# Performance work log

Measured on AMD Instinct MI355X. Metric: run time of the kernel, lower is better.

Reference implementation:

```python
import jax, jax.numpy as jnp
import numpy as np

EMBED_DIM = 1024
NUM_HEADS = 16
HEAD_DIM = EMBED_DIM // NUM_HEADS


def setup_inputs() -> dict:
    key = jax.random.key(0)
    k_x, k_wqkv, k_bqkv, k_wo, k_bo = jax.random.split(key, 5)
    B, T, C = 8, 1024, EMBED_DIM
    s = 1.0 / np.sqrt(C)
    return {
        "x": jax.random.normal(k_x, (B, T, C), dtype=jnp.float32),
        "W_qkv": jax.random.uniform(k_wqkv, (C, 3 * C), minval=-s, maxval=s, dtype=jnp.float32),
        "b_qkv": jax.random.uniform(k_bqkv, (3 * C,), minval=-s, maxval=s, dtype=jnp.float32),
        "W_out": jax.random.uniform(k_wo, (C, C), minval=-s, maxval=s, dtype=jnp.float32),
        "b_out": jax.random.uniform(k_bo, (C,), minval=-s, maxval=s, dtype=jnp.float32),
    }


def reference(x, W_qkv, b_qkv, W_out, b_out):
    B, T, C = x.shape
    H, D = NUM_HEADS, HEAD_DIM
    qkv = x @ W_qkv + b_qkv                      # [B,T,3C]
    q, k, v = jnp.split(qkv, 3, axis=-1)
    q = q.reshape(B, T, H, D).transpose(0, 2, 1, 3)  # [B,H,T,D]
    k = k.reshape(B, T, H, D).transpose(0, 2, 1, 3)
    v = v.reshape(B, T, H, D).transpose(0, 2, 1, 3)
    scores = jnp.einsum("bhqd,bhkd->bhqk", q, k) / np.sqrt(D).astype(np.float32)
    causal = jnp.tril(jnp.ones((T, T), dtype=bool))
    scores = jnp.where(causal[None, None], scores, -jnp.inf)
    attn = jax.nn.softmax(scores, axis=-1)       # dropout is identity in eval
    out = jnp.einsum("bhqk,bhkd->bhqd", attn, v)
    out = out.transpose(0, 2, 1, 3).reshape(B, T, C)
    return out @ W_out + b_out
```

## Files before the change

### kernel.cpp

```cpp
#include <hip/hip_runtime.h>
#include <hip/hip_bf16.h>
#include <cstdint>

using bf16 = __hip_bfloat16;
typedef short short8 __attribute__((ext_vector_type(8)));
typedef float floatx4 __attribute__((ext_vector_type(4)));

__device__ __forceinline__ void async_load16(const bf16* g, bf16* l) {
    __builtin_amdgcn_global_load_lds(
        (const __attribute__((address_space(1))) uint32_t*)g,
        (__attribute__((address_space(3))) uint32_t*)l, 16, 0, 0);
}

__device__ __forceinline__ uint32_t pack2(float a, float b) {
    union { bf16 h[2]; uint32_t u; } p;
    p.h[0] = __float2bfloat16(a);
    p.h[1] = __float2bfloat16(b);
    return p.u;
}

__global__ __launch_bounds__(256)
void cvt_bf16_kernel(const float* __restrict__ in, bf16* __restrict__ out) {
    const int i = (blockIdx.x * 256 + threadIdx.x) * 4;
    const float4 v = *(const float4*)(in + i);
    bf16 o[4] = {__float2bfloat16(v.x), __float2bfloat16(v.y),
                 __float2bfloat16(v.z), __float2bfloat16(v.w)};
    *(ushort4*)(out + i) = *(ushort4*)o;
}

__global__ __launch_bounds__(256)
void transpose_cvt_kernel(const float* __restrict__ in, bf16* __restrict__ out,
                          int R, int C) {
    __shared__ float tile[32][33];
    const int tx = threadIdx.x & 31, ty = threadIdx.x >> 5;
    const int c0 = blockIdx.x * 32, r0 = blockIdx.y * 32;
    #pragma unroll
    for (int i = 0; i < 32; i += 8)
        tile[ty + i][tx] = in[(size_t)(r0 + ty + i) * C + c0 + tx];
    __syncthreads();
    #pragma unroll
    for (int i = 0; i < 32; i += 8)
        out[(size_t)(c0 + ty + i) * R + r0 + tx] = __float2bfloat16(tile[tx][ty + i]);
}

template <int MODE>
__global__ __launch_bounds__(256, 2)
void gemm_bt_kernel(const bf16* __restrict__ A, const bf16* __restrict__ Bt,
                    const float* __restrict__ bias, int K,
                    bf16* __restrict__ q_ws, bf16* __restrict__ k_ws,
                    bf16* __restrict__ vt_ws, float* __restrict__ out, int N) {
    __shared__ bf16 As[128 * 32];
    __shared__ bf16 Bs[128 * 32];
    const int tid = threadIdx.x;
    const int wave = tid >> 6, lane = tid & 63;
    const int ln = lane & 15, quad = lane >> 4;
    const int wm = wave & 1, wn = wave >> 1;
    const int m0 = blockIdx.y * 128, n0 = blockIdx.x * 128;

    floatx4 acc[4][4] = {};

    for (int k0 = 0; k0 < K; k0 += 32) {
        __syncthreads();
        #pragma unroll
        for (int c = 0; c < 2; ++c) {
            const int e = (c * 256 + tid) * 8;
            async_load16(A + (size_t)(m0 + (e >> 5)) * K + k0 + (e & 31),
                         &As[(c * 256 + wave * 64) * 8]);
        }
        #pragma unroll
        for (int c = 0; c < 2; ++c) {
            const int e = (c * 256 + tid) * 8;
            async_load16(Bt + (size_t)(n0 + (e >> 5)) * K + k0 + (e & 31),
                         &Bs[(c * 256 + wave * 64) * 8]);
        }
        __syncthreads();

        short8 af[4], bfr[4];
        #pragma unroll
        for (int i = 0; i < 4; ++i) {
            af[i]  = *(const short8*)&As[(wm * 64 + i * 16 + ln) * 32 + quad * 8];
            bfr[i] = *(const short8*)&Bs[(wn * 64 + i * 16 + ln) * 32 + quad * 8];
        }
        #pragma unroll
        for (int mi = 0; mi < 4; ++mi)
            #pragma unroll
            for (int ni = 0; ni < 4; ++ni)
                acc[mi][ni] = __builtin_amdgcn_mfma_f32_16x16x32_bf16(
                    af[mi], bfr[ni], acc[mi][ni], 0, 0, 0);
    }

    #pragma unroll
    for (int ni = 0; ni < 4; ++ni) {
        const int col = n0 + wn * 64 + ni * 16 + ln;
        const float bv = bias[col];
        if (MODE == 0) {
            const int which = col >> 10;
            const int cc = col & 1023;
            const int h = cc >> 6, d = cc & 63;
            #pragma unroll
            for (int mi = 0; mi < 4; ++mi) {
                const int rowb = m0 + wm * 64 + mi * 16 + quad * 4;
                if (which == 2) {
                    const int bb = rowb >> 10, t = rowb & 1023;
                    const int tl = t & 63;
                    const int tt = (t & ~63) + ((((tl >> 3) ^ (d & 7)) << 3) | (tl & 7));
                    uint2 w2 = { pack2(acc[mi][ni][0] + bv, acc[mi][ni][1] + bv),
                                 pack2(acc[mi][ni][2] + bv, acc[mi][ni][3] + bv) };
                    *(uint2*)&vt_ws[((size_t)(bb * 16 + h) * 64 + d) * 1024 + tt] = w2;
                } else {
                    bf16* dst = (which == 0) ? q_ws : k_ws;
                    #pragma unroll
                    for (int r = 0; r < 4; ++r) {
                        const int row = rowb + r;
                        const int bb = row >> 10, t = row & 1023;
                        float v = acc[mi][ni][r] + bv;
                        if (which == 0) v *= 0.1803368801111601f;
                        const int dd = (((d >> 3) ^ (t & 7)) << 3) | (d & 7);
                        dst[((size_t)(bb * 16 + h) * 1024 + t) * 64 + dd] =
                            __float2bfloat16(v);
                    }
                }
            }
        } else {
            #pragma unroll
            for (int mi = 0; mi < 4; ++mi) {
                const int rowb = m0 + wm * 64 + mi * 16 + quad * 4;
                #pragma unroll
                for (int r = 0; r < 4; ++r)
                    out[(size_t)(rowb + r) * N + col] = acc[mi][ni][r] + bv;
            }
        }
    }
}

__global__ __launch_bounds__(256, 3)
void attn_kernel(const bf16* __restrict__ Q, const bf16* __restrict__ K,
                 const bf16* __restrict__ Vt, bf16* __restrict__ O) {
    constexpr int T = 1024;
    __shared__ bf16 Qs[128 * 64];
    __shared__ bf16 Ks[64 * 64];
    __shared__ bf16 Vts[64 * 64];
    __shared__ bf16 Ps[128 * 64];

    const int jt = blockIdx.x;
    const int q0 = jt * 128;
    const int bh = blockIdx.y;
    const int tid = threadIdx.x;
    const int wave = tid >> 6, lane = tid & 63;
    const int ln = lane & 15, quad = lane >> 4;

    const bf16* Qg = Q + (size_t)bh * T * 64 + (size_t)q0 * 64;
    const bf16* Kg = K + (size_t)bh * T * 64;
    const bf16* Vg = Vt + (size_t)bh * 64 * T;

    #pragma unroll
    for (int c = 0; c < 4; ++c)
        async_load16(Qg + (size_t)(c * 256 + tid) * 8, &Qs[(c * 256 + wave * 64) * 8]);
    __syncthreads();

    short8 bq[2][2];
    #pragma unroll
    for (int qj = 0; qj < 2; ++qj)
        #pragma unroll
        for (int ks = 0; ks < 2; ++ks) {
            const int row = wave * 32 + qj * 16 + ln;
            const int ch = (ks * 4 + quad) ^ (row & 7);
            bq[qj][ks] = *(const short8*)&Qs[row * 64 + ch * 8];
        }

    floatx4 oacc[4][2] = {};
    float rm[2] = {-1e30f, -1e30f}, rl[2] = {0.f, 0.f};
    const int qbw = q0 + wave * 32;

    const int nkt = 2 * jt + 2;
    for (int kt = 0; kt < nkt; ++kt) {
        __syncthreads();
        #pragma unroll
        for (int c = 0; c < 2; ++c)
            async_load16(Kg + (size_t)kt * 4096 + (size_t)(c * 256 + tid) * 8,
                         &Ks[(c * 256 + wave * 64) * 8]);
        #pragma unroll
        for (int c = 0; c < 2; ++c) {
            const int e = (c * 256 + tid) * 8;
            async_load16(Vg + (size_t)(e >> 6) * T + kt * 64 + (e & 63),
                         &Vts[(c * 256 + wave * 64) * 8]);
        }
        __syncthreads();

        const int k0 = kt * 64;
        if (k0 > qbw + 31) continue;
        const bool tail = (k0 + 63 > qbw);

        floatx4 sacc[4][2] = {};
        #pragma unroll
        for (int nj = 0; nj < 4; ++nj) {
            if (tail && k0 + nj * 16 > qbw + 31) continue;
            short8 ak[2];
            #pragma unroll
            for (int ks = 0; ks < 2; ++ks) {
                const int row = nj * 16 + ln;
                const int ch = (ks * 4 + quad) ^ (row & 7);
                ak[ks] = *(const short8*)&Ks[row * 64 + ch * 8];
            }
            #pragma unroll
            for (int qj = 0; qj < 2; ++qj) {
                if (tail && k0 + nj * 16 > qbw + qj * 16 + 15) continue;
                #pragma unroll
                for (int ks = 0; ks < 2; ++ks)
                    sacc[nj][qj] = __builtin_amdgcn_mfma_f32_16x16x32_bf16(
                        ak[ks], bq[qj][ks], sacc[nj][qj], 0, 0, 0);
            }
        }

        if (tail) {
            #pragma unroll
            for (int nj = 0; nj < 4; ++nj)
                #pragma unroll
                for (int qj = 0; qj < 2; ++qj) {
                    const int qq = qbw + qj * 16 + ln;
                    #pragma unroll
                    for (int r = 0; r < 4; ++r) {
                        const int kk = k0 + nj * 16 + quad * 4 + r;
                        if (kk > qq) sacc[nj][qj][r] = -1e30f;
                    }
                }
        }

        #pragma unroll
        for (int qj = 0; qj < 2; ++qj) {
            float mx = sacc[0][qj][0];
            #pragma unroll
            for (int nj = 0; nj < 4; ++nj)
                #pragma unroll
                for (int r = 0; r < 4; ++r) mx = fmaxf(mx, sacc[nj][qj][r]);
            mx = fmaxf(mx, __shfl_xor(mx, 16, 64));
            mx = fmaxf(mx, __shfl_xor(mx, 32, 64));
            const float mn = fmaxf(rm[qj], mx);
            const float alpha = exp2f(rm[qj] - mn);
            rm[qj] = mn;
            rl[qj] *= alpha;
            #pragma unroll
            for (int dt = 0; dt < 4; ++dt) oacc[dt][qj] *= alpha;
            float rs = 0.f;
            const int qrow = wave * 32 + qj * 16 + ln;
            #pragma unroll
            for (int nj = 0; nj < 4; ++nj) {
                float p[4];
                #pragma unroll
                for (int r = 0; r < 4; ++r) {
                    p[r] = exp2f(sacc[nj][qj][r] - mn);
                    rs += p[r];
                }
                const int kcol = nj * 16 + quad * 4;
                const int ch = (kcol >> 3) ^ (qrow & 7);
                uint2 w2 = { pack2(p[0], p[1]), pack2(p[2], p[3]) };
                *(uint2*)&Ps[qrow * 64 + ch * 8 + (kcol & 7)] = w2;
            }
            rl[qj] += rs;
        }

        #pragma unroll
        for (int ks4 = 0; ks4 < 2; ++ks4) {
            short8 bp[2];
            #pragma unroll
            for (int qj = 0; qj < 2; ++qj) {
                const int qrow = wave * 32 + qj * 16 + ln;
                const int ch = (ks4 * 4 + quad) ^ (qrow & 7);
                bp[qj] = *(const short8*)&Ps[qrow * 64 + ch * 8];
            }
            #pragma unroll
            for (int dt = 0; dt < 4; ++dt) {
                const int row = dt * 16 + ln;
                const int ch = (ks4 * 4 + quad) ^ (row & 7);
                const short8 av = *(const short8*)&Vts[row * 64 + ch * 8];
                #pragma unroll
                for (int qj = 0; qj < 2; ++qj)
                    oacc[dt][qj] = __builtin_amdgcn_mfma_f32_16x16x32_bf16(
                        av, bp[qj], oacc[dt][qj], 0, 0, 0);
            }
        }
    }

    const int b = bh >> 4, h = bh & 15;
    #pragma unroll
    for (int qj = 0; qj < 2; ++qj) {
        float l = rl[qj];
        l += __shfl_xor(l, 16, 64);
        l += __shfl_xor(l, 32, 64);
        const float inv = 1.0f / l;
        const int t = q0 + wave * 32 + qj * 16 + ln;
        const size_t rowb = ((size_t)b * 1024 + t) * 1024 + h * 64;
        #pragma unroll
        for (int dt = 0; dt < 4; ++dt) {
            uint2 w2 = { pack2(oacc[dt][qj][0] * inv, oacc[dt][qj][1] * inv),
                         pack2(oacc[dt][qj][2] * inv, oacc[dt][qj][3] * inv) };
            *(uint2*)&O[rowb + dt * 16 + quad * 4] = w2;
        }
    }
}

extern "C" void kernel_launch(void* const* d_in, const int* in_sizes, int n_in,
                              void* d_out, int out_size, void* d_ws, size_t ws_size,
                              hipStream_t stream) {
    const float* x     = (const float*)d_in[0];
    const float* W_qkv = (const float*)d_in[1];
    const float* b_qkv = (const float*)d_in[2];
    const float* W_out = (const float*)d_in[3];
    const float* b_out = (const float*)d_in[4];
    float* out = (float*)d_out;

    char* ws = (char*)d_ws;
    const size_t MB = 1u << 20;
    bf16* x_bf   = (bf16*)(ws + 0);
    bf16* wqkv_t = (bf16*)(ws + 16 * MB);
    bf16* wout_t = (bf16*)(ws + 22 * MB);
    bf16* q_ws   = (bf16*)(ws + 24 * MB);
    bf16* k_ws   = (bf16*)(ws + 40 * MB);
    bf16* vt_ws  = (bf16*)(ws + 56 * MB);
    bf16* ao_ws  = (bf16*)(ws + 72 * MB);

    cvt_bf16_kernel<<<8192, 256, 0, stream>>>(x, x_bf);
    transpose_cvt_kernel<<<dim3(96, 32), 256, 0, stream>>>(W_qkv, wqkv_t, 1024, 3072);
    transpose_cvt_kernel<<<dim3(32, 32), 256, 0, stream>>>(W_out, wout_t, 1024, 1024);

    gemm_bt_kernel<0><<<dim3(24, 64), 256, 0, stream>>>(
        x_bf, wqkv_t, b_qkv, 1024, q_ws, k_ws, vt_ws, nullptr, 3072);

    attn_kernel<<<dim3(8, 128), 256, 0, stream>>>(q_ws, k_ws, vt_ws, ao_ws);

    gemm_bt_kernel<1><<<dim3(8, 64), 256, 0, stream>>>(
        ao_ws, wout_t, b_out, 1024, nullptr, nullptr, nullptr, out, 1024);
}
```

Baseline: 286.2 us.

## Pair causal query tiles per block and double-buffer K/V tiles in attention

Each attention block now handles two query tiles, jt and 7-jt, so the causal work per block is balanced and the grid is halved. K and V tiles are double-buffered so the next tile's async global-to-LDS load is issued before computing on the current one, leaving one barrier per iteration. The Q staging buffer is reused for the P tile, which offsets the extra LDS used by the second K/V buffers. With fewer blocks, there is less parallelism to hide latency, and each block runs twice as long.

```diff
diff --git a/kernel.cpp b/kernel.cpp
--- a/kernel.cpp
+++ b/kernel.cpp
@@ -137,164 +137,183 @@
 void attn_kernel(const bf16* __restrict__ Q, const bf16* __restrict__ K,
                  const bf16* __restrict__ Vt, bf16* __restrict__ O) {
     constexpr int T = 1024;
-    __shared__ bf16 Qs[128 * 64];
-    __shared__ bf16 Ks[64 * 64];
-    __shared__ bf16 Vts[64 * 64];
-    __shared__ bf16 Ps[128 * 64];
-
-    const int jt = blockIdx.x;
-    const int q0 = jt * 128;
+    __shared__ bf16 QPs[128 * 64];
+    __shared__ bf16 Ks[2][64 * 64];
+    __shared__ bf16 Vts[2][64 * 64];
+
     const int bh = blockIdx.y;
     const int tid = threadIdx.x;
     const int wave = tid >> 6, lane = tid & 63;
     const int ln = lane & 15, quad = lane >> 4;
 
-    const bf16* Qg = Q + (size_t)bh * T * 64 + (size_t)q0 * 64;
     const bf16* Kg = K + (size_t)bh * T * 64;
     const bf16* Vg = Vt + (size_t)bh * 64 * T;
+    const int b = bh >> 4, h = bh & 15;
 
     #pragma unroll
-    for (int c = 0; c < 4; ++c)
-        async_load16(Qg + (size_t)(c * 256 + tid) * 8, &Qs[(c * 256 + wave * 64) * 8]);
-    __syncthreads();
-
-    short8 bq[2][2];
-    #pragma unroll
-    for (int qj = 0; qj < 2; ++qj)
-        #pragma unroll
-        for (int ks = 0; ks < 2; ++ks) {
-            const int row = wave * 32 + qj * 16 + ln;
-            const int ch = (ks * 4 + quad) ^ (row & 7);
-            bq[qj][ks] = *(const short8*)&Qs[row * 64 + ch * 8];
-        }
-
-    floatx4 oacc[4][2] = {};
-    float rm[2] = {-1e30f, -1e30f}, rl[2] = {0.f, 0.f};
-    const int qbw = q0 + wave * 32;
-
-    const int nkt = 2 * jt + 2;
-    for (int kt = 0; kt < nkt; ++kt) {
-        __syncthreads();
+    for (int phase = 0; phase < 2; ++phase) {
+        const int jt = phase ? 7 - blockIdx.x : blockIdx.x;
+        const int q0 = jt * 128;
+        const int nkt = 2 * jt + 2;
+
+        const bf16* Qg = Q + (size_t)bh * T * 64 + (size_t)q0 * 64;
+        #pragma unroll
+        for (int c = 0; c < 4; ++c)
+            async_load16(Qg + (size_t)(c * 256 + tid) * 8,
+                         &QPs[(c * 256 + wave * 64) * 8]);
         #pragma unroll
         for (int c = 0; c < 2; ++c)
-            async_load16(Kg + (size_t)kt * 4096 + (size_t)(c * 256 + tid) * 8,
-                         &Ks[(c * 256 + wave * 64) * 8]);
+            async_load16(Kg + (size_t)(c * 256 + tid) * 8,
+                         &Ks[0][(c * 256 + wave * 64) * 8]);
         #pragma unroll
         for (int c = 0; c < 2; ++c) {
             const int e = (c * 256 + tid) * 8;
-            async_load16(Vg + (size_t)(e >> 6) * T + kt * 64 + (e & 63),
-                         &Vts[(c * 256 + wave * 64) * 8]);
+            async_load16(Vg + (size_t)(e >> 6) * T + (e & 63),
+                         &Vts[0][(c * 256 + wave * 64) * 8]);
         }
         __syncthreads();
 
-        const int k0 = kt * 64;
-        if (k0 > qbw + 31) continue;
-        const bool tail = (k0 + 63 > qbw);
-
-        floatx4 sacc[4][2] = {};
-        #pragma unroll
-        for (int nj = 0; nj < 4; ++nj) {
-            if (tail && k0 + nj * 16 > qbw + 31) continue;
-            short8 ak[2];
+        short8 bq[2][2];
+        #pragma unroll
+        for (int qj = 0; qj < 2; ++qj)
             #pragma unroll
             for (int ks = 0; ks < 2; ++ks) {
-                const int row = nj * 16 + ln;
+                const int row = wave * 32 + qj * 16 + ln;
                 const int ch = (ks * 4 + quad) ^ (row & 7);
-                ak[ks] = *(const short8*)&Ks[row * 64 + ch * 8];
-            }
-            #pragma unroll
-            for (int qj = 0; qj < 2; ++qj) {
-                if (tail && k0 + nj * 16 > qbw + qj * 16 + 15) continue;
-                #pragma unroll
-                for (int ks = 0; ks < 2; ++ks)
-                    sacc[nj][qj] = __builtin_amdgcn_mfma_f32_16x16x32_bf16(
-                        ak[ks], bq[qj][ks], sacc[nj][qj], 0, 0, 0);
-            }
-        }
-
-        if (tail) {
-            #pragma unroll
-            for (int nj = 0; nj < 4; ++nj)
+                bq[qj][ks] = *(const short8*)&QPs[row * 64 + ch * 8];
+            }
+
+        floatx4 oacc[4][2] = {};
+        float rm[2] = {-1e30f, -1e30f}, rl[2] = {0.f, 0.f};
+        const int qbw = q0 + wave * 32;
+
+        for (int kt = 0; kt < nkt; ++kt) {
+            const int cur = kt & 1;
+            if (kt + 1 < nkt) {
+                const int nxt = cur ^ 1;
+                #pragma unroll
+                for (int c = 0; c < 2; ++c)
+                    async_load16(Kg + (size_t)(kt + 1) * 4096 + (size_t)(c * 256 + tid) * 8,
+                                 &Ks[nxt][(c * 256 + wave * 64) * 8]);
+                #pragma unroll
+                for (int c = 0; c < 2; ++c) {
+                    const int e = (c * 256 + tid) * 8;
+                    async_load16(Vg + (size_t)(e >> 6) * T + (kt + 1) * 64 + (e & 63),
+                                 &Vts[nxt][(c * 256 + wave * 64) * 8]);
+                }
+            }
+
+            const int k0 = kt * 64;
+            if (k0 <= qbw + 31) {
+                const bool tail = (k0 + 63 > qbw);
+
+                floatx4 sacc[4][2] = {};
+                #pragma unroll
+                for (int nj = 0; nj < 4; ++nj) {
+                    if (tail && k0 + nj * 16 > qbw + 31) continue;
+                    short8 ak[2];
+                    #pragma unroll
+                    for (int ks = 0; ks < 2; ++ks) {
+                        const int row = nj * 16 + ln;
+                        const int ch = (ks * 4 + quad) ^ (row & 7);
+                        ak[ks] = *(const short8*)&Ks[cur][row * 64 + ch * 8];
+                    }
+                    #pragma unroll
+                    for (int qj = 0; qj < 2; ++qj) {
+                        if (tail && k0 + nj * 16 > qbw + qj * 16 + 15) continue;
+                        #pragma unroll
+                        for (int ks = 0; ks < 2; ++ks)
+                            sacc[nj][qj] = __builtin_amdgcn_mfma_f32_16x16x32_bf16(
+                                ak[ks], bq[qj][ks], sacc[nj][qj], 0, 0, 0);
+                    }
+                }
+
+                if (tail) {
+                    #pragma unroll
+                    for (int nj = 0; nj < 4; ++nj)
+                        #pragma unroll
+                        for (int qj = 0; qj < 2; ++qj) {
+                            const int qq = qbw + qj * 16 + ln;
+                            #pragma unroll
+                            for (int r = 0; r < 4; ++r) {
+                                const int kk = k0 + nj * 16 + quad * 4 + r;
+                                if (kk > qq) sacc[nj][qj][r] = -1e30f;
+                            }
+                        }
+                }
+
                 #pragma unroll
                 for (int qj = 0; qj < 2; ++qj) {
-                    const int qq = qbw + qj * 16 + ln;
-                    #pragma unroll
-                    for (int r = 0; r < 4; ++r) {
-                        const int kk = k0 + nj * 16 + quad * 4 + r;
-                        if (kk > qq) sacc[nj][qj][r] = -1e30f;
-                    }
-                }
+                    float mx = sacc[0][qj][0];
+                    #pragma unroll
+                    for (int nj = 0; nj < 4; ++nj)
+                        #pragma unroll
+                        for (int r = 0; r < 4; ++r) mx = fmaxf(mx, sacc[nj][qj][r]);
+                    mx = fmaxf(mx, __shfl_xor(mx, 16, 64));
+                    mx = fmaxf(mx, __shfl_xor(mx, 32, 64));
+                    const float mn = fmaxf(rm[qj], mx);
+                    const float alpha = exp2f(rm[qj] - mn);
+                    rm[qj] = mn;
+                    rl[qj] *= alpha;
+                    #pragma unroll
+                    for (int dt = 0; dt < 4; ++dt) oacc[dt][qj] *= alpha;
+                    float rs = 0.f;
+                    const int qrow = wave * 32 + qj * 16 + ln;
+                    #pragma unroll
+                    for (int nj = 0; nj < 4; ++nj) {
+                        float p[4];
+                        #pragma unroll
+                        for (int r = 0; r < 4; ++r) {
+                            p[r] = exp2f(sacc[nj][qj][r] - mn);
+                            rs += p[r];
+                        }
+                        const int kcol = nj * 16 + quad * 4;
+                        const int ch = (kcol >> 3) ^ (qrow & 7);
+                        uint2 w2 = { pack2(p[0], p[1]), pack2(p[2], p[3]) };
+                        *(uint2*)&QPs[qrow * 64 + ch * 8 + (kcol & 7)] = w2;
+                    }
+                    rl[qj] += rs;
+                }
+
+                #pragma unroll
+                for (int ks4 = 0; ks4 < 2; ++ks4) {
+                    short8 bp[2];
+                    #pragma unroll
+                    for (int qj = 0; qj < 2; ++qj) {
+                        const int qrow = wave * 32 + qj * 16 + ln;
+                        const int ch = (ks4 * 4 + quad) ^ (qrow & 7);
+                        bp[qj] = *(const short8*)&QPs[qrow * 64 + ch * 8];
+                    }
+                    #pragma unroll
+                    for (int dt = 0; dt < 4; ++dt) {
+                        const int row = dt * 16 + ln;
+                        const int ch = (ks4 * 4 + quad) ^ (row & 7);
+                        const short8 av = *(const short8*)&Vts[cur][row * 64 + ch * 8];
+                        #pragma unroll
+                        for (int qj = 0; qj < 2; ++qj)
+                            oacc[dt][qj] = __builtin_amdgcn_mfma_f32_16x16x32_bf16(
+                                av, bp[qj], oacc[dt][qj], 0, 0, 0);
+                    }
+                }
+            }
+
+            __syncthreads();
         }
 
         #pragma unroll
         for (int qj = 0; qj < 2; ++qj) {
-            float mx = sacc[0][qj][0];
-            #pragma unroll
-            for (int nj = 0; nj < 4; ++nj)
-                #pragma unroll
-                for (int r = 0; r < 4; ++r) mx = fmaxf(mx, sacc[nj][qj][r]);
-            mx = fmaxf(mx, __shfl_xor(mx, 16, 64));
-            mx = fmaxf(mx, __shfl_xor(mx, 32, 64));
-            const float mn = fmaxf(rm[qj], mx);
-            const float alpha = exp2f(rm[qj] - mn);
-            rm[qj] = mn;
-            rl[qj] *= alpha;
-            #pragma unroll
-            for (int dt = 0; dt < 4; ++dt) oacc[dt][qj] *= alpha;
-            float rs = 0.f;
-            const int qrow = wave * 32 + qj * 16 + ln;
-            #pragma unroll
-            for (int nj = 0; nj < 4; ++nj) {
-                float p[4];
-                #pragma unroll
-                for (int r = 0; r < 4; ++r) {
-                    p[r] = exp2f(sacc[nj][qj][r] - mn);
-                    rs += p[r];
-                }
-                const int kcol = nj * 16 + quad * 4;
-                const int ch = (kcol >> 3) ^ (qrow & 7);
-                uint2 w2 = { pack2(p[0], p[1]), pack2(p[2], p[3]) };
-                *(uint2*)&Ps[qrow * 64 + ch * 8 + (kcol & 7)] = w2;
-            }
-            rl[qj] += rs;
-        }
-
-        #pragma unroll
-        for (int ks4 = 0; ks4 < 2; ++ks4) {
-            short8 bp[2];
-            #pragma unroll
-            for (int qj = 0; qj < 2; ++qj) {
-                const int qrow = wave * 32 + qj * 16 + ln;
-                const int ch = (ks4 * 4 + quad) ^ (qrow & 7);
-                bp[qj] = *(const short8*)&Ps[qrow * 64 + ch * 8];
-            }
+            float l = rl[qj];
+            l += __shfl_xor(l, 16, 64);
+            l += __shfl_xor(l, 32, 64);
+            const float inv = 1.0f / l;
+            const int t = q0 + wave * 32 + qj * 16 + ln;
+            const size_t rowb = ((size_t)b * 1024 + t) * 1024 + h * 64;
             #pragma unroll
             for (int dt = 0; dt < 4; ++dt) {
-                const int row = dt * 16 + ln;
-                const int ch = (ks4 * 4 + quad) ^ (row & 7);
-                const short8 av = *(const short8*)&Vts[row * 64 + ch * 8];
-                #pragma unroll
-                for (int qj = 0; qj < 2; ++qj)
-                    oacc[dt][qj] = __builtin_amdgcn_mfma_f32_16x16x32_bf16(
-                        av, bp[qj], oacc[dt][qj], 0, 0, 0);
-            }
-        }
-    }
-
-    const int b = bh >> 4, h = bh & 15;
-    #pragma unroll
-    for (int qj = 0; qj < 2; ++qj) {
-        float l = rl[qj];
-        l += __shfl_xor(l, 16, 64);
-        l += __shfl_xor(l, 32, 64);
-        const float inv = 1.0f / l;
-        const int t = q0 + wave * 32 + qj * 16 + ln;
-        const size_t rowb = ((size_t)b * 1024 + t) * 1024 + h * 64;
-        #pragma unroll
-        for (int dt = 0; dt < 4; ++dt) {
-            uint2 w2 = { pack2(oacc[dt][qj][0] * inv, oacc[dt][qj][1] * inv),
-                         pack2(oacc[dt][qj][2] * inv, oacc[dt][qj][3] * inv) };
-            *(uint2*)&O[rowb + dt * 16 + quad * 4] = w2;
+                uint2 w2 = { pack2(oacc[dt][qj][0] * inv, oacc[dt][qj][1] * inv),
+                             pack2(oacc[dt][qj][2] * inv, oacc[dt][qj][3] * inv) };
+                *(uint2*)&O[rowb + dt * 16 + quad * 4] = w2;
+            }
         }
     }
 }
@@ -326,7 +345,7 @@
     gemm_bt_kernel<0><<<dim3(24, 64), 256, 0, stream>>>(
         x_bf, wqkv_t, b_qkv, 1024, q_ws, k_ws, vt_ws, nullptr, 3072);
 
-    attn_kernel<<<dim3(8, 128), 256, 0, stream>>>(q_ws, k_ws, vt_ws, ao_ws);
+    attn_kernel<<<dim3(4, 128), 256, 0, stream>>>(q_ws, k_ws, vt_ws, ao_ws);
 
     gemm_bt_kernel<1><<<dim3(8, 64), 256, 0, stream>>>(
         ao_ws, wout_t, b_out, 1024, nullptr, nullptr, nullptr, out, 1024);
```

Result: faster. 252.2 us (-11.9%).
